# Kernel optimization log

Hardware: AMD Instinct MI355X
Metric: run time of the kernel (lower is better)

Reference implementation:

```python
import jax, jax.numpy as jnp
import numpy as np

D_MODEL, D_HEAD, N_HEAD, H, W = 256, 32, 8, 24, 24
B = 16
GN_GROUPS = 16
GN_EPS = 1e-5
SCALE = 1.0 / (D_HEAD ** 0.5)


def setup_inputs() -> dict:
    key = jax.random.key(0)
    ks = jax.random.split(key, 8)
    rn = lambda k, shape, s=1.0: jax.random.normal(k, shape, jnp.float32) * s
    return {
        "x": rn(ks[0], (B, D_MODEL, H, W)),
        "qkv_w": rn(ks[1], (3 * N_HEAD * D_HEAD, D_MODEL), 0.05),  # 1x1 conv kernel (squeezed)
        "qkv_b": jnp.zeros((3 * N_HEAD * D_HEAD,), jnp.float32),
        "rh_k": rn(ks[2], (2 * H - 1, N_HEAD, D_HEAD), SCALE),
        "rw_k": rn(ks[3], (2 * W - 1, N_HEAD, D_HEAD), SCALE),
        "rh_v": rn(ks[4], (1, 2 * H - 1, N_HEAD, D_HEAD), SCALE),
        "rw_v": rn(ks[5], (1, 2 * W - 1, N_HEAD, D_HEAD), SCALE),
        "fc_w": rn(ks[6], (D_MODEL, N_HEAD * D_HEAD), 0.05),  # 1x1 conv kernel (squeezed)
        "fc_b": jnp.zeros((D_MODEL,), jnp.float32),
        "gn_w": jnp.ones((D_MODEL,), jnp.float32),
        "gn_b": jnp.zeros((D_MODEL,), jnp.float32),
    }


def rel_shift(x, qlen):
    # x: (t, L, ...) -> (t, qlen, ...), Transformer-XL relative shift (pure reshape)
    t, L = x.shape[0], x.shape[1]
    rest = x.shape[2:]
    zero_pad = jnp.zeros((t, 1) + rest, x.dtype)
    x_padded = jnp.concatenate([zero_pad, x], axis=1)          # (t, L+1, ...)
    x_padded = x_padded.reshape((L + 1, t) + rest)
    return x_padded[1:].reshape((t, L) + rest)[:, :qlen]


def rel_shift_2d(xh, xw, h, w):
    xh = rel_shift(xh, h)                                       # (t, h, ...)
    xw = rel_shift(xw, w)                                       # (t, w, ...)
    tile_h = (1, w) + (1,) * (xh.ndim - 2)
    tile_w = (1, h) + (1,) * (xw.ndim - 2)
    return jnp.tile(xh, tile_h) + jnp.tile(xw, tile_w)          # (t, t, ...)


def _forward(x, qkv_w, qkv_b, rh_k, rw_k, rh_v, rw_v, fc_w, fc_b, gn_w, gn_b):
    b, c, h, w = x.shape
    t = h * w
    n, d = N_HEAD, D_HEAD

    # 1x1 conv qkv -> (b, 3n, d, t); chunk along axis 1 exactly like torch.chunk(dim=1)
    xf = x.reshape(b, c, t)
    qkv = jnp.einsum('oc,bct->bot', qkv_w, xf) + qkv_b[None, :, None]
    qkv = qkv.reshape(b, 3 * n, d, t)
    q, k, v = jnp.split(qkv, 3, axis=1)                         # each (b, n, d, t)

    ac = jnp.einsum('bndi,bndj->bnij', q, k)                    # (b, n, t, t)
    bd_h = jnp.einsum('bndi,jnd->ijbn', q, rh_k)                # (t, 2h-1, b, n)
    bd_w = jnp.einsum('bndi,jnd->ijbn', q, rw_k)                # (t, 2w-1, b, n)
    bd = rel_shift_2d(bd_h, bd_w, h, w)                         # (t, t, b, n)
    bd = bd.transpose(2, 3, 0, 1)                               # (b, n, t, t)

    # NOTE: faithful to the source, softmax is over dim=1 (the head axis)
    attn = jax.nn.softmax((ac + bd) * SCALE, axis=1)

    pos_emb_v = rel_shift_2d(jnp.tile(rh_v, (t, 1, 1, 1)),
                             jnp.tile(rw_v, (t, 1, 1, 1)), h, w)  # (t, t, n, d)

    out = jnp.einsum('bnij,bndj->bndi', attn, v) \
        + jnp.einsum('bnij,ijnd->bndi', attn, pos_emb_v)        # (b, n, d, t)
    out = out.reshape(b, n * d, t)

    y = jnp.einsum('oc,bct->bot', fc_w, out) + fc_b[None, :, None]  # (b, c, t)
    y = y.reshape(b, c, h, w) + x                               # residual

    # GroupNorm(16, c)
    yg = y.reshape(b, GN_GROUPS, c // GN_GROUPS * h * w)
    mu = jnp.mean(yg, axis=2, keepdims=True)
    var = jnp.var(yg, axis=2, keepdims=True)
    yn = ((yg - mu) / jnp.sqrt(var + GN_EPS)).reshape(b, c, h, w)
    return yn * gn_w[None, :, None, None] + gn_b[None, :, None, None]


def reference(x, qkv_w, qkv_b, rh_k, rw_k, rh_v, rw_v, fc_w, fc_b, gn_w, gn_b):
    return _forward(x, qkv_w, qkv_b, rh_k, rw_k, rh_v, rw_v, fc_w, fc_b, gn_w, gn_b)
```

## Files before the change

kernel.cpp:

```cpp
#include <hip/hip_runtime.h>
#include <math.h>

#define BB 16
#define CHN 256
#define TT 576
#define NHD 8
#define DHD 32
#define SCALE_F 0.17677669529663687f

__device__ __forceinline__ int SW(int p, int d) {
    return ((((d >> 2) ^ (p & 7)) << 2) | (d & 3));
}

__global__ __launch_bounds__(256) void qkv_gemm_k(const float* __restrict__ x,
                                                  const float* __restrict__ w,
                                                  const float* __restrict__ bias,
                                                  float* __restrict__ out) {
    __shared__ float ws[32 * 260];
    __shared__ float xs[32 * 36];
    int orig = blockIdx.x;
    int wg = (orig & 7) * 96 + (orig >> 3);
    int b = wg / 48;
    int rem = wg % 48;
    int it = rem / 3, oh = rem % 3;
    int o0 = oh * 256, i0 = it * 36;
    int tid = threadIdx.x;
    int og = tid >> 2, itg = tid & 3;

    float acc[4][9];
#pragma unroll
    for (int r = 0; r < 4; ++r)
#pragma unroll
        for (int s = 0; s < 9; ++s) acc[r][s] = 0.f;

    for (int kt = 0; kt < 8; ++kt) {
        for (int idx4 = tid; idx4 < 2048; idx4 += 256) {
            int oo = idx4 >> 3, kc4 = (idx4 & 7) * 4;
            const float4 v = *reinterpret_cast<const float4*>(&w[(o0 + oo) * 256 + kt * 32 + kc4]);
            ws[(kc4 + 0) * 260 + oo] = v.x;
            ws[(kc4 + 1) * 260 + oo] = v.y;
            ws[(kc4 + 2) * 260 + oo] = v.z;
            ws[(kc4 + 3) * 260 + oo] = v.w;
        }
        for (int idx4 = tid; idx4 < 288; idx4 += 256) {
            int kc = idx4 / 9, ii4 = idx4 % 9;
            const float4 v = *reinterpret_cast<const float4*>(&x[(b * 256 + kt * 32 + kc) * 576 + i0 + ii4 * 4]);
            *reinterpret_cast<float4*>(&xs[kc * 36 + ii4 * 4]) = v;
        }
        __syncthreads();
#pragma unroll 8
        for (int kc = 0; kc < 32; ++kc) {
            float4 wr = *reinterpret_cast<const float4*>(&ws[kc * 260 + og * 4]);
            float xv[9];
#pragma unroll
            for (int s = 0; s < 9; ++s) xv[s] = xs[kc * 36 + itg * 9 + s];
#pragma unroll
            for (int s = 0; s < 9; ++s) {
                acc[0][s] += wr.x * xv[s];
                acc[1][s] += wr.y * xv[s];
                acc[2][s] += wr.z * xv[s];
                acc[3][s] += wr.w * xv[s];
            }
        }
        __syncthreads();
    }
#pragma unroll
    for (int r = 0; r < 4; ++r) {
        int o = o0 + og * 4 + r;
        float bb = bias[o];
#pragma unroll
        for (int s = 0; s < 9; ++s)
            out[(b * 768 + o) * 576 + i0 + itg * 9 + s] = acc[r][s] + bb;
    }
}

__global__ __launch_bounds__(256) void attn_k(const float* __restrict__ qkv,
                                              const float* __restrict__ rh_k,
                                              const float* __restrict__ rw_k,
                                              const float* __restrict__ rh_v,
                                              const float* __restrict__ rw_v,
                                              float* __restrict__ att_out) {
    __shared__ float qs[12288];
    __shared__ float kvs[12288];
    __shared__ float bds[6912];
    __shared__ float ats[6912];

    int orig = blockIdx.x;
    int wg = (orig & 7) * 32 + (orig >> 3);
    int b = wg >> 4, it = wg & 15;
    int i0 = it * 36;
    int tid = threadIdx.x;
    const float* qb = qkv + (size_t)b * 768 * 576;

    for (int idx4 = tid; idx4 < 3072; idx4 += 256) {
        int o = idx4 / 12, iw4 = (idx4 % 12) * 4;
        int n = o >> 5, d = o & 31;
        int gi = i0 + iw4;
        float4 v;
        if (gi + 3 < 576) {
            v = *reinterpret_cast<const float4*>(&qb[o * 576 + gi]);
        } else {
            v.x = (gi + 0 < 576) ? qb[o * 576 + gi + 0] : 0.f;
            v.y = (gi + 1 < 576) ? qb[o * 576 + gi + 1] : 0.f;
            v.z = (gi + 2 < 576) ? qb[o * 576 + gi + 2] : 0.f;
            v.w = (gi + 3 < 576) ? qb[o * 576 + gi + 3] : 0.f;
        }
        qs[n * 1536 + (iw4 + 0) * 32 + SW(iw4 + 0, d)] = v.x;
        qs[n * 1536 + (iw4 + 1) * 32 + SW(iw4 + 1, d)] = v.y;
        qs[n * 1536 + (iw4 + 2) * 32 + SW(iw4 + 2, d)] = v.z;
        qs[n * 1536 + (iw4 + 3) * 32 + SW(iw4 + 3, d)] = v.w;
    }
    for (int idx = tid; idx < 12032; idx += 256) {
        int j = idx >> 8, nd = idx & 255;
        kvs[j * 260 + nd] = rh_k[idx] + rw_k[idx];
    }
    __syncthreads();

    int n1 = tid >> 5;
    int g1 = tid & 31, ig1 = g1 >> 3, jg1 = g1 & 7;
    int dg = (tid >> 2) & 7, ig2 = tid & 3;
    int d0 = dg * 4, ib = ig2 * 9;

#pragma unroll
    for (int r = 0; r < 9; ++r) {
        int i_loc = ig1 * 9 + r;
        int f0 = 576 + 47 * (i0 + i_loc);
#pragma unroll
        for (int s = 0; s < 3; ++s) {
            int c = jg1 * 3 + s;
            int f = f0 + c;
            int j = f % 48;
            float val = 0.f;
            if (j > 0) {
                int isl = f / 48 - i0;
                int bq = n1 * 1536 + isl * 32;
                int swz = isl & 7;
                int br = (j - 1) * 260 + n1 * 32;
#pragma unroll
                for (int dq = 0; dq < 8; ++dq) {
                    float4 qv = *reinterpret_cast<const float4*>(&qs[bq + (((dq ^ swz)) << 2)]);
                    float4 rv = *reinterpret_cast<const float4*>(&kvs[br + dq * 4]);
                    val += qv.x * rv.x + qv.y * rv.y + qv.z * rv.z + qv.w * rv.w;
                }
            }
            bds[n1 * 864 + i_loc * 24 + c] = val;
        }
    }
    __syncthreads();

    float cs[4][8];
#pragma unroll
    for (int k = 0; k < 4; ++k)
#pragma unroll
        for (int nn = 0; nn < 8; ++nn) cs[k][nn] = 0.f;
    float acc[4][9];
#pragma unroll
    for (int r = 0; r < 4; ++r)
#pragma unroll
        for (int s = 0; s < 9; ++s) acc[r][s] = 0.f;

    for (int tt = 0; tt < 24; ++tt) {
        const float* kb = qb + 256 * 576 + tt * 24;
        const float* vb = qb + 512 * 576 + tt * 24;
        for (int idx4 = tid; idx4 < 1536; idx4 += 256) {
            int o = idx4 / 6, c4 = (idx4 % 6) * 4;
            int n = o >> 5, d = o & 31;
            float4 kv = *reinterpret_cast<const float4*>(&kb[o * 576 + c4]);
            float4 vv = *reinterpret_cast<const float4*>(&vb[o * 576 + c4]);
            int base = n * 768;
            kvs[base + (c4 + 0) * 32 + SW(c4 + 0, d)] = kv.x;
            kvs[base + (c4 + 1) * 32 + SW(c4 + 1, d)] = kv.y;
            kvs[base + (c4 + 2) * 32 + SW(c4 + 2, d)] = kv.z;
            kvs[base + (c4 + 3) * 32 + SW(c4 + 3, d)] = kv.w;
            kvs[6144 + base + (c4 + 0) * 32 + SW(c4 + 0, d)] = vv.x;
            kvs[6144 + base + (c4 + 1) * 32 + SW(c4 + 1, d)] = vv.y;
            kvs[6144 + base + (c4 + 2) * 32 + SW(c4 + 2, d)] = vv.z;
            kvs[6144 + base + (c4 + 3) * 32 + SW(c4 + 3, d)] = vv.w;
        }
        __syncthreads();

        {
            float a[9][3];
#pragma unroll
            for (int r = 0; r < 9; ++r)
#pragma unroll
                for (int s = 0; s < 3; ++s)
                    a[r][s] = bds[n1 * 864 + (ig1 * 9 + r) * 24 + jg1 * 3 + s];
#pragma unroll
            for (int dq = 0; dq < 8; ++dq) {
                float4 qv[9], kv[3];
#pragma unroll
                for (int r = 0; r < 9; ++r) {
                    int iw = ig1 * 9 + r;
                    qv[r] = *reinterpret_cast<const float4*>(&qs[n1 * 1536 + iw * 32 + ((dq ^ (iw & 7)) << 2)]);
                }
#pragma unroll
                for (int s = 0; s < 3; ++s) {
                    int c = jg1 * 3 + s;
                    kv[s] = *reinterpret_cast<const float4*>(&kvs[n1 * 768 + c * 32 + ((dq ^ (c & 7)) << 2)]);
                }
#pragma unroll
                for (int r = 0; r < 9; ++r)
#pragma unroll
                    for (int s = 0; s < 3; ++s)
                        a[r][s] += qv[r].x * kv[s].x + qv[r].y * kv[s].y +
                                   qv[r].z * kv[s].z + qv[r].w * kv[s].w;
            }
#pragma unroll
            for (int r = 0; r < 9; ++r)
#pragma unroll
                for (int s = 0; s < 3; ++s)
                    ats[n1 * 864 + (ig1 * 9 + r) * 24 + jg1 * 3 + s] = a[r][s] * SCALE_F;
        }
        __syncthreads();

#pragma unroll
        for (int k = 0; k < 4; ++k) {
            int p = k * 256 + tid;
            if (p < 864) {
                float xv[8];
#pragma unroll
                for (int nn = 0; nn < 8; ++nn) xv[nn] = ats[nn * 864 + p];
                float m = xv[0];
#pragma unroll
                for (int nn = 1; nn < 8; ++nn) m = fmaxf(m, xv[nn]);
                float e[8], ssum = 0.f;
#pragma unroll
                for (int nn = 0; nn < 8; ++nn) { e[nn] = __expf(xv[nn] - m); ssum += e[nn]; }
                float inv = 1.0f / ssum;
#pragma unroll
                for (int nn = 0; nn < 8; ++nn) {
                    float aa = e[nn] * inv;
                    ats[nn * 864 + p] = aa;
                    cs[k][nn] += aa;
                }
            }
        }
        __syncthreads();

#pragma unroll 4
        for (int c = 0; c < 24; ++c) {
            float4 vv = *reinterpret_cast<const float4*>(&kvs[6144 + n1 * 768 + c * 32 + ((dg ^ (c & 7)) << 2)]);
            const float* abase = &ats[n1 * 864 + ib * 24 + c];
#pragma unroll
            for (int s = 0; s < 9; ++s) {
                float pv = abase[s * 24];
                acc[0][s] += vv.x * pv;
                acc[1][s] += vv.y * pv;
                acc[2][s] += vv.z * pv;
                acc[3][s] += vv.w * pv;
            }
        }
        __syncthreads();
    }

#pragma unroll
    for (int k = 0; k < 4; ++k) {
        int p = k * 256 + tid;
        if (p < 864) {
#pragma unroll
            for (int nn = 0; nn < 8; ++nn) ats[nn * 864 + p] = cs[k][nn];
        }
    }
    for (int idx = tid; idx < 12032; idx += 256) {
        int j = idx >> 8, nd = idx & 255;
        qs[j * 260 + nd] = rh_v[idx] + rw_v[idx];
    }
    __syncthreads();

#pragma unroll
    for (int s = 0; s < 9; ++s) {
        int i_loc = ib + s;
        int f0 = 576 + 47 * (i0 + i_loc);
#pragma unroll 4
        for (int c = 0; c < 24; ++c) {
            int f = f0 + c;
            int j = f % 48;
            if (j > 0) {
                float wv = ats[n1 * 864 + i_loc * 24 + c];
                float4 rr = *reinterpret_cast<const float4*>(&qs[(j - 1) * 260 + n1 * 32 + d0]);
                acc[0][s] += wv * rr.x;
                acc[1][s] += wv * rr.y;
                acc[2][s] += wv * rr.z;
                acc[3][s] += wv * rr.w;
            }
        }
    }

#pragma unroll
    for (int r = 0; r < 4; ++r)
#pragma unroll
        for (int s = 0; s < 9; ++s)
            att_out[((size_t)b * 256 + n1 * 32 + d0 + r) * 576 + i0 + ib + s] = acc[r][s];
}

__global__ __launch_bounds__(256) void fc_k(const float* __restrict__ att,
                                            const float* __restrict__ w,
                                            const float* __restrict__ bias,
                                            const float* __restrict__ x,
                                            float* __restrict__ y) {
    __shared__ float ws[32 * 260];
    __shared__ float as[32 * 36];
    int orig = blockIdx.x;
    int wg = (orig & 7) * 32 + (orig >> 3);
    int b = wg >> 4, it = wg & 15;
    int i0 = it * 36;
    int tid = threadIdx.x;
    int og = tid >> 2, itg = tid & 3;

    float acc[4][9];
#pragma unroll
    for (int r = 0; r < 4; ++r)
#pragma unroll
        for (int s = 0; s < 9; ++s) acc[r][s] = 0.f;

    for (int kt = 0; kt < 8; ++kt) {
        for (int idx4 = tid; idx4 < 2048; idx4 += 256) {
            int oo = idx4 >> 3, kc4 = (idx4 & 7) * 4;
            const float4 v = *reinterpret_cast<const float4*>(&w[oo * 256 + kt * 32 + kc4]);
            ws[(kc4 + 0) * 260 + oo] = v.x;
            ws[(kc4 + 1) * 260 + oo] = v.y;
            ws[(kc4 + 2) * 260 + oo] = v.z;
            ws[(kc4 + 3) * 260 + oo] = v.w;
        }
        for (int idx4 = tid; idx4 < 288; idx4 += 256) {
            int kc = idx4 / 9, ii4 = idx4 % 9;
            const float4 v = *reinterpret_cast<const float4*>(&att[(b * 256 + kt * 32 + kc) * 576 + i0 + ii4 * 4]);
            *reinterpret_cast<float4*>(&as[kc * 36 + ii4 * 4]) = v;
        }
        __syncthreads();
#pragma unroll 8
        for (int kc = 0; kc < 32; ++kc) {
            float4 wr = *reinterpret_cast<const float4*>(&ws[kc * 260 + og * 4]);
            float xv[9];
#pragma unroll
            for (int s = 0; s < 9; ++s) xv[s] = as[kc * 36 + itg * 9 + s];
#pragma unroll
            for (int s = 0; s < 9; ++s) {
                acc[0][s] += wr.x * xv[s];
                acc[1][s] += wr.y * xv[s];
                acc[2][s] += wr.z * xv[s];
                acc[3][s] += wr.w * xv[s];
            }
        }
        __syncthreads();
    }
#pragma unroll
    for (int r = 0; r < 4; ++r) {
        int o = og * 4 + r;
        float bb = bias[o];
#pragma unroll
        for (int s = 0; s < 9; ++s) {
            int gidx = (b * 256 + o) * 576 + i0 + itg * 9 + s;
            y[gidx] = acc[r][s] + bb + x[gidx];
        }
    }
}

__global__ __launch_bounds__(256) void gn_k(float* __restrict__ y,
                                            const float* __restrict__ gw,
                                            const float* __restrict__ gb) {
    __shared__ double psum[4], psq[4];
    __shared__ float stat[2];
    int b = blockIdx.x >> 4, grp = blockIdx.x & 15;
    size_t base = ((size_t)b * 256 + grp * 16) * 576;
    int tid = threadIdx.x;
    int lane = tid & 63, wid = tid >> 6;

    float4 vals[9];
    double s = 0.0, s2 = 0.0;
#pragma unroll
    for (int k = 0; k < 9; ++k) {
        float4 v = *reinterpret_cast<const float4*>(&y[base + (size_t)(k * 256 + tid) * 4]);
        vals[k] = v;
        s += (double)v.x + (double)v.y + (double)v.z + (double)v.w;
        s2 += (double)v.x * v.x + (double)v.y * v.y + (double)v.z * v.z + (double)v.w * v.w;
    }
#pragma unroll
    for (int off = 32; off > 0; off >>= 1) {
        s += __shfl_down(s, off);
        s2 += __shfl_down(s2, off);
    }
    if (lane == 0) { psum[wid] = s; psq[wid] = s2; }
    __syncthreads();
    if (tid == 0) {
        double ts = psum[0] + psum[1] + psum[2] + psum[3];
        double tq = psq[0] + psq[1] + psq[2] + psq[3];
        double mean = ts * (1.0 / 9216.0);
        double var = tq * (1.0 / 9216.0) - mean * mean;
        stat[0] = (float)mean;
        stat[1] = (float)(1.0 / sqrt(var + 1e-5));
    }
    __syncthreads();
    float mf = stat[0], rstd = stat[1];
#pragma unroll
    for (int k = 0; k < 9; ++k) {
        int idx4 = k * 256 + tid;
        int ch = grp * 16 + idx4 / 144;
        float wv = gw[ch], bv = gb[ch];
        float4 v = vals[k];
        float4 r;
        r.x = (v.x - mf) * rstd * wv + bv;
        r.y = (v.y - mf) * rstd * wv + bv;
        r.z = (v.z - mf) * rstd * wv + bv;
        r.w = (v.w - mf) * rstd * wv + bv;
        *reinterpret_cast<float4*>(&y[base + (size_t)idx4 * 4]) = r;
    }
}

extern "C" void kernel_launch(void* const* d_in, const int* in_sizes, int n_in,
                              void* d_out, int out_size, void* d_ws, size_t ws_size,
                              hipStream_t stream) {
    const float* x     = (const float*)d_in[0];
    const float* qkv_w = (const float*)d_in[1];
    const float* qkv_b = (const float*)d_in[2];
    const float* rh_k  = (const float*)d_in[3];
    const float* rw_k  = (const float*)d_in[4];
    const float* rh_v  = (const float*)d_in[5];
    const float* rw_v  = (const float*)d_in[6];
    const float* fc_w  = (const float*)d_in[7];
    const float* fc_b  = (const float*)d_in[8];
    const float* gn_w  = (const float*)d_in[9];
    const float* gn_b  = (const float*)d_in[10];
    float* out = (float*)d_out;

    float* qkv = (float*)d_ws;
    float* att = qkv + 7077888;

    qkv_gemm_k<<<768, 256, 0, stream>>>(x, qkv_w, qkv_b, qkv);
    attn_k<<<256, 256, 0, stream>>>(qkv, rh_k, rw_k, rh_v, rw_v, att);
    fc_k<<<256, 256, 0, stream>>>(att, fc_w, fc_b, x, out);
    gn_k<<<256, 256, 0, stream>>>(out, gn_w, gn_b);
}
```

Measured before the change: 415.7 us.

## Double attention block width to 512 threads with split-d reductions and register-prefetched K/V

The attention kernel now runs 512 threads per block. Each head gets 64 lanes that split the d reduction of QK^T in halves and combine them with shuffles, and split the PV columns in halves, combined with xor-1 shuffles. The next K/V tile is prefetched into registers during the current tile's compute, bias terms stay in registers instead of a shared buffer, and the softmax pass covers positions in two strided chunks. This aims to raise parallelism and hide global load latency on a grid of only 256 blocks, at the cost of more register pressure, extra shuffles and redundant qv loads.

Result: slower. 1.135 ms (+173.1%).

```diff
diff --git a/kernel.cpp b/kernel.cpp
--- a/kernel.cpp
+++ b/kernel.cpp
@@ -74,15 +74,14 @@
     }
 }
 
-__global__ __launch_bounds__(256) void attn_k(const float* __restrict__ qkv,
-                                              const float* __restrict__ rh_k,
-                                              const float* __restrict__ rw_k,
-                                              const float* __restrict__ rh_v,
-                                              const float* __restrict__ rw_v,
-                                              float* __restrict__ att_out) {
+__global__ __launch_bounds__(512, 2) void attn_k(const float* __restrict__ qkv,
+                                                 const float* __restrict__ rh_k,
+                                                 const float* __restrict__ rw_k,
+                                                 const float* __restrict__ rh_v,
+                                                 const float* __restrict__ rw_v,
+                                                 float* __restrict__ att_out) {
     __shared__ float qs[12288];
     __shared__ float kvs[12288];
-    __shared__ float bds[6912];
     __shared__ float ats[6912];
 
     int orig = blockIdx.x;
@@ -92,7 +91,15 @@
     int tid = threadIdx.x;
     const float* qb = qkv + (size_t)b * 768 * 576;
 
-    for (int idx4 = tid; idx4 < 3072; idx4 += 256) {
+    int n1 = tid >> 6;
+    int lane = tid & 63;
+    int slot = lane & 31, dh = lane >> 5;
+    int ig1 = slot >> 3, jg1 = slot & 7;
+    int dg = lane >> 3;
+    int ig2 = (lane >> 1) & 3, ch = lane & 1;
+    int d0 = dg * 4, ib = ig2 * 9;
+
+    for (int idx4 = tid; idx4 < 3072; idx4 += 512) {
         int o = idx4 / 12, iw4 = (idx4 % 12) * 4;
         int n = o >> 5, d = o & 31;
         int gi = i0 + iw4;
@@ -110,17 +117,26 @@
         qs[n * 1536 + (iw4 + 2) * 32 + SW(iw4 + 2, d)] = v.z;
         qs[n * 1536 + (iw4 + 3) * 32 + SW(iw4 + 3, d)] = v.w;
     }
-    for (int idx = tid; idx < 12032; idx += 256) {
+    for (int idx = tid; idx < 12032; idx += 512) {
         int j = idx >> 8, nd = idx & 255;
         kvs[j * 260 + nd] = rh_k[idx] + rw_k[idx];
     }
+
+    float4 kvf[3], vvf[3];
+    {
+        const float* kb = qb + 256 * 576;
+        const float* vb = qb + 512 * 576;
+#pragma unroll
+        for (int k = 0; k < 3; ++k) {
+            int idx4 = tid + k * 512;
+            int o = idx4 / 6, c4 = (idx4 % 6) * 4;
+            kvf[k] = *reinterpret_cast<const float4*>(&kb[o * 576 + c4]);
+            vvf[k] = *reinterpret_cast<const float4*>(&vb[o * 576 + c4]);
+        }
+    }
     __syncthreads();
 
-    int n1 = tid >> 5;
-    int g1 = tid & 31, ig1 = g1 >> 3, jg1 = g1 & 7;
-    int dg = (tid >> 2) & 7, ig2 = tid & 3;
-    int d0 = dg * 4, ib = ig2 * 9;
-
+    float bdreg[9][3];
 #pragma unroll
     for (int r = 0; r < 9; ++r) {
         int i_loc = ig1 * 9 + r;
@@ -135,22 +151,22 @@
                 int isl = f / 48 - i0;
                 int bq = n1 * 1536 + isl * 32;
                 int swz = isl & 7;
-                int br = (j - 1) * 260 + n1 * 32;
-#pragma unroll
-                for (int dq = 0; dq < 8; ++dq) {
-                    float4 qv = *reinterpret_cast<const float4*>(&qs[bq + (((dq ^ swz)) << 2)]);
+                int br = (j - 1) * 260 + n1 * 32 + dh * 16;
+#pragma unroll
+                for (int dq = 0; dq < 4; ++dq) {
+                    int dqq = dh * 4 + dq;
+                    float4 qv = *reinterpret_cast<const float4*>(&qs[bq + ((dqq ^ swz) << 2)]);
                     float4 rv = *reinterpret_cast<const float4*>(&kvs[br + dq * 4]);
                     val += qv.x * rv.x + qv.y * rv.y + qv.z * rv.z + qv.w * rv.w;
                 }
             }
-            bds[n1 * 864 + i_loc * 24 + c] = val;
-        }
-    }
-    __syncthreads();
-
-    float cs[4][8];
-#pragma unroll
-    for (int k = 0; k < 4; ++k)
+            bdreg[r][s] = val;
+        }
+    }
+
+    float cs[2][8];
+#pragma unroll
+    for (int k = 0; k < 2; ++k)
 #pragma unroll
         for (int nn = 0; nn < 8; ++nn) cs[k][nn] = 0.f;
     float acc[4][9];
@@ -160,22 +176,32 @@
         for (int s = 0; s < 9; ++s) acc[r][s] = 0.f;
 
     for (int tt = 0; tt < 24; ++tt) {
-        const float* kb = qb + 256 * 576 + tt * 24;
-        const float* vb = qb + 512 * 576 + tt * 24;
-        for (int idx4 = tid; idx4 < 1536; idx4 += 256) {
+        __syncthreads();
+#pragma unroll
+        for (int k = 0; k < 3; ++k) {
+            int idx4 = tid + k * 512;
             int o = idx4 / 6, c4 = (idx4 % 6) * 4;
             int n = o >> 5, d = o & 31;
-            float4 kv = *reinterpret_cast<const float4*>(&kb[o * 576 + c4]);
-            float4 vv = *reinterpret_cast<const float4*>(&vb[o * 576 + c4]);
             int base = n * 768;
-            kvs[base + (c4 + 0) * 32 + SW(c4 + 0, d)] = kv.x;
-            kvs[base + (c4 + 1) * 32 + SW(c4 + 1, d)] = kv.y;
-            kvs[base + (c4 + 2) * 32 + SW(c4 + 2, d)] = kv.z;
-            kvs[base + (c4 + 3) * 32 + SW(c4 + 3, d)] = kv.w;
-            kvs[6144 + base + (c4 + 0) * 32 + SW(c4 + 0, d)] = vv.x;
-            kvs[6144 + base + (c4 + 1) * 32 + SW(c4 + 1, d)] = vv.y;
-            kvs[6144 + base + (c4 + 2) * 32 + SW(c4 + 2, d)] = vv.z;
-            kvs[6144 + base + (c4 + 3) * 32 + SW(c4 + 3, d)] = vv.w;
+            kvs[base + (c4 + 0) * 32 + SW(c4 + 0, d)] = kvf[k].x;
+            kvs[base + (c4 + 1) * 32 + SW(c4 + 1, d)] = kvf[k].y;
+            kvs[base + (c4 + 2) * 32 + SW(c4 + 2, d)] = kvf[k].z;
+            kvs[base + (c4 + 3) * 32 + SW(c4 + 3, d)] = kvf[k].w;
+            kvs[6144 + base + (c4 + 0) * 32 + SW(c4 + 0, d)] = vvf[k].x;
+            kvs[6144 + base + (c4 + 1) * 32 + SW(c4 + 1, d)] = vvf[k].y;
+            kvs[6144 + base + (c4 + 2) * 32 + SW(c4 + 2, d)] = vvf[k].z;
+            kvs[6144 + base + (c4 + 3) * 32 + SW(c4 + 3, d)] = vvf[k].w;
+        }
+        if (tt + 1 < 24) {
+            const float* kb = qb + 256 * 576 + (tt + 1) * 24;
+            const float* vb = qb + 512 * 576 + (tt + 1) * 24;
+#pragma unroll
+            for (int k = 0; k < 3; ++k) {
+                int idx4 = tid + k * 512;
+                int o = idx4 / 6, c4 = (idx4 % 6) * 4;
+                kvf[k] = *reinterpret_cast<const float4*>(&kb[o * 576 + c4]);
+                vvf[k] = *reinterpret_cast<const float4*>(&vb[o * 576 + c4]);
+            }
         }
         __syncthreads();
 
@@ -184,20 +210,20 @@
 #pragma unroll
             for (int r = 0; r < 9; ++r)
 #pragma unroll
-                for (int s = 0; s < 3; ++s)
-                    a[r][s] = bds[n1 * 864 + (ig1 * 9 + r) * 24 + jg1 * 3 + s];
-#pragma unroll
-            for (int dq = 0; dq < 8; ++dq) {
+                for (int s = 0; s < 3; ++s) a[r][s] = bdreg[r][s];
+#pragma unroll
+            for (int dq = 0; dq < 4; ++dq) {
+                int dqq = dh * 4 + dq;
                 float4 qv[9], kv[3];
 #pragma unroll
                 for (int r = 0; r < 9; ++r) {
                     int iw = ig1 * 9 + r;
-                    qv[r] = *reinterpret_cast<const float4*>(&qs[n1 * 1536 + iw * 32 + ((dq ^ (iw & 7)) << 2)]);
+                    qv[r] = *reinterpret_cast<const float4*>(&qs[n1 * 1536 + iw * 32 + ((dqq ^ (iw & 7)) << 2)]);
                 }
 #pragma unroll
                 for (int s = 0; s < 3; ++s) {
                     int c = jg1 * 3 + s;
-                    kv[s] = *reinterpret_cast<const float4*>(&kvs[n1 * 768 + c * 32 + ((dq ^ (c & 7)) << 2)]);
+                    kv[s] = *reinterpret_cast<const float4*>(&kvs[n1 * 768 + c * 32 + ((dqq ^ (c & 7)) << 2)]);
                 }
 #pragma unroll
                 for (int r = 0; r < 9; ++r)
@@ -210,68 +236,105 @@
             for (int r = 0; r < 9; ++r)
 #pragma unroll
                 for (int s = 0; s < 3; ++s)
-                    ats[n1 * 864 + (ig1 * 9 + r) * 24 + jg1 * 3 + s] = a[r][s] * SCALE_F;
-        }
-        __syncthreads();
-
-#pragma unroll
-        for (int k = 0; k < 4; ++k) {
-            int p = k * 256 + tid;
-            if (p < 864) {
-                float xv[8];
-#pragma unroll
-                for (int nn = 0; nn < 8; ++nn) xv[nn] = ats[nn * 864 + p];
-                float m = xv[0];
-#pragma unroll
-                for (int nn = 1; nn < 8; ++nn) m = fmaxf(m, xv[nn]);
-                float e[8], ssum = 0.f;
-#pragma unroll
-                for (int nn = 0; nn < 8; ++nn) { e[nn] = __expf(xv[nn] - m); ssum += e[nn]; }
-                float inv = 1.0f / ssum;
+                    a[r][s] += __shfl_xor(a[r][s], 32);
+            if (dh == 0) {
+#pragma unroll
+                for (int r = 0; r < 9; ++r)
+#pragma unroll
+                    for (int s = 0; s < 3; ++s)
+                        ats[n1 * 864 + (ig1 * 9 + r) * 24 + jg1 * 3 + s] = a[r][s] * SCALE_F;
+            }
+        }
+        __syncthreads();
+
+        {
+            int p = tid;
+            float xv[8];
+#pragma unroll
+            for (int nn = 0; nn < 8; ++nn) xv[nn] = ats[nn * 864 + p];
+            float m = xv[0];
+#pragma unroll
+            for (int nn = 1; nn < 8; ++nn) m = fmaxf(m, xv[nn]);
+            float ssum = 0.f;
+#pragma unroll
+            for (int nn = 0; nn < 8; ++nn) { xv[nn] = __expf(xv[nn] - m); ssum += xv[nn]; }
+            float inv = 1.0f / ssum;
+#pragma unroll
+            for (int nn = 0; nn < 8; ++nn) {
+                float aa = xv[nn] * inv;
+                ats[nn * 864 + p] = aa;
+                cs[0][nn] += aa;
+            }
+            if (tid < 352) {
+                int p2 = 512 + tid;
+                float yv[8];
+#pragma unroll
+                for (int nn = 0; nn < 8; ++nn) yv[nn] = ats[nn * 864 + p2];
+                float m2 = yv[0];
+#pragma unroll
+                for (int nn = 1; nn < 8; ++nn) m2 = fmaxf(m2, yv[nn]);
+                float ss2 = 0.f;
+#pragma unroll
+                for (int nn = 0; nn < 8; ++nn) { yv[nn] = __expf(yv[nn] - m2); ss2 += yv[nn]; }
+                float inv2 = 1.0f / ss2;
 #pragma unroll
                 for (int nn = 0; nn < 8; ++nn) {
-                    float aa = e[nn] * inv;
-                    ats[nn * 864 + p] = aa;
-                    cs[k][nn] += aa;
+                    float aa = yv[nn] * inv2;
+                    ats[nn * 864 + p2] = aa;
+                    cs[1][nn] += aa;
                 }
             }
         }
         __syncthreads();
 
-#pragma unroll 4
-        for (int c = 0; c < 24; ++c) {
-            float4 vv = *reinterpret_cast<const float4*>(&kvs[6144 + n1 * 768 + c * 32 + ((dg ^ (c & 7)) << 2)]);
-            const float* abase = &ats[n1 * 864 + ib * 24 + c];
+#pragma unroll
+        for (int ccq = 0; ccq < 3; ++ccq) {
+            int ccbase = ch * 12 + ccq * 4;
+            float4 vv[4];
+#pragma unroll
+            for (int j = 0; j < 4; ++j) {
+                int c2 = ccbase + j;
+                vv[j] = *reinterpret_cast<const float4*>(&kvs[6144 + n1 * 768 + c2 * 32 + ((dg ^ (c2 & 7)) << 2)]);
+            }
 #pragma unroll
             for (int s = 0; s < 9; ++s) {
-                float pv = abase[s * 24];
-                acc[0][s] += vv.x * pv;
-                acc[1][s] += vv.y * pv;
-                acc[2][s] += vv.z * pv;
-                acc[3][s] += vv.w * pv;
-            }
-        }
-        __syncthreads();
-    }
-
-#pragma unroll
-    for (int k = 0; k < 4; ++k) {
-        int p = k * 256 + tid;
-        if (p < 864) {
-#pragma unroll
-            for (int nn = 0; nn < 8; ++nn) ats[nn * 864 + p] = cs[k][nn];
-        }
-    }
-    for (int idx = tid; idx < 12032; idx += 256) {
+                float4 pv = *reinterpret_cast<const float4*>(&ats[n1 * 864 + (ib + s) * 24 + ccbase]);
+                acc[0][s] += vv[0].x * pv.x + vv[1].x * pv.y + vv[2].x * pv.z + vv[3].x * pv.w;
+                acc[1][s] += vv[0].y * pv.x + vv[1].y * pv.y + vv[2].y * pv.z + vv[3].y * pv.w;
+                acc[2][s] += vv[0].z * pv.x + vv[1].z * pv.y + vv[2].z * pv.z + vv[3].z * pv.w;
+                acc[3][s] += vv[0].w * pv.x + vv[1].w * pv.y + vv[2].w * pv.z + vv[3].w * pv.w;
+            }
+        }
+    }
+    __syncthreads();
+
+#pragma unroll
+    for (int r = 0; r < 4; ++r)
+#pragma unroll
+        for (int s = 0; s < 9; ++s)
+            acc[r][s] += __shfl_xor(acc[r][s], 1);
+
+    {
+        int p = tid;
+#pragma unroll
+        for (int nn = 0; nn < 8; ++nn) ats[nn * 864 + p] = cs[0][nn];
+        if (tid < 352) {
+            int p2 = 512 + tid;
+#pragma unroll
+            for (int nn = 0; nn < 8; ++nn) ats[nn * 864 + p2] = cs[1][nn];
+        }
+    }
+    for (int idx = tid; idx < 12032; idx += 512) {
         int j = idx >> 8, nd = idx & 255;
         qs[j * 260 + nd] = rh_v[idx] + rw_v[idx];
     }
     __syncthreads();
 
-#pragma unroll
-    for (int s = 0; s < 9; ++s) {
+    int s_lo = ch ? 5 : 0, s_hi = ch ? 9 : 5;
+    for (int s = s_lo; s < s_hi; ++s) {
         int i_loc = ib + s;
         int f0 = 576 + 47 * (i0 + i_loc);
+        float a0 = acc[0][s], a1 = acc[1][s], a2 = acc[2][s], a3 = acc[3][s];
 #pragma unroll 4
         for (int c = 0; c < 24; ++c) {
             int f = f0 + c;
@@ -279,19 +342,18 @@
             if (j > 0) {
                 float wv = ats[n1 * 864 + i_loc * 24 + c];
                 float4 rr = *reinterpret_cast<const float4*>(&qs[(j - 1) * 260 + n1 * 32 + d0]);
-                acc[0][s] += wv * rr.x;
-                acc[1][s] += wv * rr.y;
-                acc[2][s] += wv * rr.z;
-                acc[3][s] += wv * rr.w;
-            }
-        }
-    }
-
-#pragma unroll
-    for (int r = 0; r < 4; ++r)
-#pragma unroll
-        for (int s = 0; s < 9; ++s)
-            att_out[((size_t)b * 256 + n1 * 32 + d0 + r) * 576 + i0 + ib + s] = acc[r][s];
+                a0 += wv * rr.x;
+                a1 += wv * rr.y;
+                a2 += wv * rr.z;
+                a3 += wv * rr.w;
+            }
+        }
+        size_t ob = ((size_t)b * 256 + n1 * 32 + d0) * 576 + i0 + i_loc;
+        att_out[ob] = a0;
+        att_out[ob + 576] = a1;
+        att_out[ob + 1152] = a2;
+        att_out[ob + 1728] = a3;
+    }
 }
 
 __global__ __launch_bounds__(256) void fc_k(const float* __restrict__ att,
@@ -428,7 +490,7 @@
     float* att = qkv + 7077888;
 
     qkv_gemm_k<<<768, 256, 0, stream>>>(x, qkv_w, qkv_b, qkv);
-    attn_k<<<256, 256, 0, stream>>>(qkv, rh_k, rw_k, rh_v, rw_v, att);
+    attn_k<<<256, 512, 0, stream>>>(qkv, rh_k, rw_k, rh_v, rw_v, att);
     fc_k<<<256, 256, 0, stream>>>(att, fc_w, fc_b, x, out);
     gn_k<<<256, 256, 0, stream>>>(out, gn_w, gn_b);
 }
```
